# Kernel optimization log

Hardware: AMD Instinct MI355X
Metric: run time of the kernel (lower is better)

The kernel has to match this reference:

```python
import jax, jax.numpy as jnp
import numpy as np


def setup_inputs() -> dict:
    key = jax.random.key(0)
    k1, k2 = jax.random.split(key)
    x = jax.random.normal(k1, (32, 64, 64, 64), dtype=jnp.float32)
    codebook = jax.random.normal(k2, (1024, 64), dtype=jnp.float32)
    return {"x": x, "codebook": codebook}


def reference(x, codebook):
    # x: (B, D, H, W)  codebook: (K, D)
    B, D = x.shape[0], x.shape[1]
    spatial = x.shape[2:]
    flat = x.reshape(B, D, -1).transpose(0, 2, 1)  # (B, N, D)
    dot = jnp.einsum("bnd,kd->bnk", flat, codebook)
    cb_norm = jnp.sum(codebook * codebook, axis=-1)  # (K,)
    indices = jnp.argmin(cb_norm[None, None, :] - 2.0 * dot, axis=-1)  # (B, N)
    quantized = codebook[indices]  # (B, N, D) gather
    out = quantized.transpose(0, 2, 1).reshape(x.shape)
    return out, indices.reshape((B,) + spatial)
```

## Files before the change

kernel.cpp:

```cpp
#include <hip/hip_runtime.h>


typedef _Float16 f16x8 __attribute__((ext_vector_type(8)));
typedef float    f32x4 __attribute__((ext_vector_type(4)));

#define VQ_D    64
#define VQ_HW   4096
#define VQ_NPOS 131072
#define SC      2048.0f
#define EPS_Q   24
#define WS_CBN  65536
#define WS_CNQ  66560
#define WS_CBT  67584
#define WS_CNT  133120
#define WS_LIST 133124

__global__ __launch_bounds__(256)
void vq_prep(const float* __restrict__ cb, float* __restrict__ ws)
{
    const int tid = threadIdx.x;
    const int blk = blockIdx.x;
    if (blk < 64) {
        const int it   = blk * 256 + tid;
        const int ct   = it >> 8;
        const int s    = (it >> 6) & 3;
        const int lane = it & 63;
        const int ks   = s & 1, isR = s >> 1;
        const int n    = ct * 16 + (lane & 15);
        const int k0   = ks * 32 + (lane >> 4) * 8;
        const float* src = cb + n * 64 + k0;
        f16x8 o;
        #pragma unroll
        for (int j = 0; j < 8; ++j) {
            const float b = src[j];
            const _Float16 bh = (_Float16)b;
            o[j] = isR ? (_Float16)((b - (float)bh) * (-2.0f * SC))
                       : (_Float16)(-2.0f * (float)bh);
        }
        ((f16x8*)ws)[it] = o;
    } else if (blk < 128) {
        const int it = (blk - 64) * 256 + tid;
        const int k = it >> 4, j4 = it & 15;
        ((float4*)(ws + WS_CBT))[j4 * 1024 + k] = ((const float4*)cb)[it];
    } else {
        const int k = (blk - 128) * 256 + tid;
        const float4* row = (const float4*)(cb + k * 64);
        float a0 = 0.f, a1 = 0.f, a2 = 0.f, a3 = 0.f;
        #pragma unroll
        for (int j = 0; j < 16; ++j) {
            const float4 c = row[j];
            a0 = fmaf(c.x, c.x, a0); a1 = fmaf(c.y, c.y, a1);
            a2 = fmaf(c.z, c.z, a2); a3 = fmaf(c.w, c.w, a3);
        }
        const float cn = (a0 + a1) + (a2 + a3);
        ws[WS_CBN + k] = cn;
        ws[WS_CNQ + k] = cn * 2048.0f;
        if (k == 0) ((int*)ws)[WS_CNT] = 0;
    }
}

#define GLOAD_LDS(GP, LP)                                                     \
    __builtin_amdgcn_global_load_lds(                                         \
        (const __attribute__((address_space(1))) unsigned int*)(GP),          \
        (__attribute__((address_space(3))) unsigned int*)(LP), 16, 0, 0)

#define STAGE2(CK, BOFF)                                                      \
    {                                                                         \
        const char* gs_ = (const char*)ws + (size_t)(CK) * 8192               \
                          + wv * 2048 + lane * 16;                            \
        char* ld_ = (char*)bbuf + (BOFF) + wv * 2048;                         \
        GLOAD_LDS(gs_, ld_);                                                  \
        GLOAD_LDS(gs_ + 1024, ld_ + 1024);                                    \
    }

#define CT_BODY(BOFF, CI, CTG)                                                \
    {                                                                         \
        const f16x8 B0 = *(const f16x8*)(lp + (BOFF) + (CI) * 4096);          \
        const f16x8 B1 = *(const f16x8*)(lp + (BOFF) + (CI) * 4096 + 1024);   \
        const f16x8 R0 = *(const f16x8*)(lp + (BOFF) + (CI) * 4096 + 2048);   \
        const f16x8 R1 = *(const f16x8*)(lp + (BOFF) + (CI) * 4096 + 3072);   \
        const float cvq = cnq_lds[(CTG) * 16 + m];                            \
        const f32x4 Ci = {cvq, cvq, cvq, cvq};                                \
        f32x4 pa[4], pb[4];                                                   \
        __builtin_amdgcn_s_setprio(1);                                        \
        _Pragma("unroll")                                                     \
        for (int tl = 0; tl < 4; ++tl) {                                      \
            pa[tl] = __builtin_amdgcn_mfma_f32_16x16x32_f16(Ak[tl][0], B0, Ci,    0,0,0); \
            pb[tl] = __builtin_amdgcn_mfma_f32_16x16x32_f16(Ak[tl][1], B1, zero4, 0,0,0); \
        }                                                                     \
        _Pragma("unroll")                                                     \
        for (int tl = 0; tl < 4; ++tl) {                                      \
            pa[tl] = __builtin_amdgcn_mfma_f32_16x16x32_f16(Ah[tl][0], R0, pa[tl], 0,0,0); \
            pb[tl] = __builtin_amdgcn_mfma_f32_16x16x32_f16(Ah[tl][1], R1, pb[tl], 0,0,0); \
        }                                                                     \
        _Pragma("unroll")                                                     \
        for (int tl = 0; tl < 4; ++tl) {                                      \
            pa[tl] = __builtin_amdgcn_mfma_f32_16x16x32_f16(Ra[tl][0], B0, pa[tl], 0,0,0); \
            pb[tl] = __builtin_amdgcn_mfma_f32_16x16x32_f16(Ra[tl][1], B1, pb[tl], 0,0,0); \
        }                                                                     \
        __builtin_amdgcn_s_setprio(0);                                        \
        const int cbase_ = (CTG) * 16 + m;                                    \
        _Pragma("unroll")                                                     \
        for (int tl = 0; tl < 4; ++tl)                                        \
            _Pragma("unroll")                                                 \
            for (int r = 0; r < 4; ++r) {                                     \
                const float q_ = pa[tl][r] + pb[tl][r];                       \
                const int k_ = ((int)q_ << 10) | cbase_;                      \
                int md_;                                                      \
                asm("v_med3_i32 %0, %1, %2, %3"                               \
                    : "=v"(md_) : "v"(k_), "v"(d1[tl][r]), "v"(d2[tl][r]));   \
                d2[tl][r] = md_;                                              \
                d1[tl][r] = (k_ < d1[tl][r]) ? k_ : d1[tl][r];                \
            }                                                                 \
    }

#define ITER_T(VMSTR, DOSTAGE, T)                                             \
    {                                                                         \
        asm volatile("s_waitcnt " VMSTR ::: "memory");                        \
        __builtin_amdgcn_s_barrier();                                         \
        if (DOSTAGE) STAGE2((T) + 3, (((T) + 3) & 3) * 8192)                  \
        const int base_ = ((T) & 3) * 8192;                                   \
        CT_BODY(base_, 0, (T) * 2)                                            \
        CT_BODY(base_, 1, (T) * 2 + 1)                                        \
    }

__global__ __launch_bounds__(256, 2)
void vq_main(const float* __restrict__ x,
             const float* __restrict__ cb,
             float* __restrict__ ws,
             float* __restrict__ out,
             float* __restrict__ idx_out)
{
    __shared__ f16x8 bbuf[4 * 512];
    __shared__ float cnq_lds[1024];
    __shared__ int   sk[256];
    __shared__ int   smg[256];

    const int tid  = threadIdx.x;
    const int lane = tid & 63;
    const int wv   = tid >> 6;
    const int m    = lane & 15;
    const int q    = lane >> 4;

    const int p0 = blockIdx.x * 256;
    const int b  = p0 >> 12;
    const int n0 = p0 & (VQ_HW - 1);
    const float* xw = x + (size_t)b * (VQ_D * VQ_HW) + n0 + wv * 64;

    STAGE2(0, 0)
    STAGE2(1, 8192)
    STAGE2(2, 16384)

    ((float4*)cnq_lds)[tid] = ((const float4*)(ws + WS_CNQ))[tid];

    f16x8 Ah[4][2], Ak[4][2], Ra[4][2];
    #pragma unroll
    for (int tl = 0; tl < 4; ++tl)
        #pragma unroll
        for (int ks = 0; ks < 2; ++ks) {
            f16x8 h8, k8, r8;
            #pragma unroll
            for (int j = 0; j < 8; ++j) {
                const float v = xw[(size_t)(ks * 32 + q * 8 + j) * VQ_HW + tl * 16 + m];
                const _Float16 vh = (_Float16)v;
                h8[j] = vh;
                k8[j] = (_Float16)((float)vh * 2048.0f);
                r8[j] = (_Float16)((v - (float)vh) * SC);
            }
            Ah[tl][ks] = h8; Ak[tl][ks] = k8; Ra[tl][ks] = r8;
        }

    int d1[4][4], d2[4][4];
    #pragma unroll
    for (int tl = 0; tl < 4; ++tl)
        #pragma unroll
        for (int r = 0; r < 4; ++r) { d1[tl][r] = 0x7FFFFFFF; d2[tl][r] = 0x7FFFFFFF; }

    const f32x4 zero4 = {0.f, 0.f, 0.f, 0.f};
    const char* lp = (const char*)bbuf + lane * 16;

    __syncthreads();

    for (int t = 0; t < 29; ++t)
        ITER_T("vmcnt(4)", 1, t)
    ITER_T("vmcnt(4)", 0, 29)
    ITER_T("vmcnt(2)", 0, 30)
    ITER_T("vmcnt(0)", 0, 31)

    #pragma unroll
    for (int off = 1; off < 16; off <<= 1)
        #pragma unroll
        for (int tl = 0; tl < 4; ++tl)
            #pragma unroll
            for (int r = 0; r < 4; ++r) {
                const int od1 = __shfl_xor(d1[tl][r], off, 64);
                const int od2 = __shfl_xor(d2[tl][r], off, 64);
                const int mx  = (d1[tl][r] > od1) ? d1[tl][r] : od1;
                const int mn2 = (d2[tl][r] < od2) ? d2[tl][r] : od2;
                d2[tl][r] = (mx < mn2) ? mx : mn2;
                d1[tl][r] = (d1[tl][r] < od1) ? d1[tl][r] : od1;
            }

    if (m == 0) {
        #pragma unroll
        for (int tl = 0; tl < 4; ++tl)
            #pragma unroll
            for (int r = 0; r < 4; ++r) {
                const int li = wv * 64 + tl * 16 + q * 4 + r;
                sk[li]  = d1[tl][r] & 1023;
                smg[li] = (d2[tl][r] >> 10) - (d1[tl][r] >> 10);
            }
    }
    __syncthreads();

    const int bk = sk[tid];
    idx_out[p0 + tid] = (float)bk;
    if (smg[tid] < EPS_Q) {
        const int slot = atomicAdd((int*)ws + WS_CNT, 1);
        ((int*)ws)[WS_LIST + slot] = p0 + tid;
    }
    const float4* cr = (const float4*)(cb + (size_t)bk * VQ_D);
    float* ob = out + (size_t)b * (VQ_D * VQ_HW) + n0 + tid;
    #pragma unroll
    for (int d4 = 0; d4 < 16; ++d4) {
        const float4 v = cr[d4];
        ob[(size_t)(d4 * 4 + 0) * VQ_HW] = v.x;
        ob[(size_t)(d4 * 4 + 1) * VQ_HW] = v.y;
        ob[(size_t)(d4 * 4 + 2) * VQ_HW] = v.z;
        ob[(size_t)(d4 * 4 + 3) * VQ_HW] = v.w;
    }
}

__global__ __launch_bounds__(64)
void vq_rescan(const float* __restrict__ x,
               const float* __restrict__ cb,
               const float* __restrict__ ws,
               float* __restrict__ out,
               float* __restrict__ idx_out)
{
    __shared__ float xs[VQ_D];
    const int lane = threadIdx.x;
    const int cnt  = ((const int*)ws)[WS_CNT];
    const int* list = (const int*)ws + WS_LIST;
    const float*  cnb  = ws + WS_CBN;
    const float4* cbT4 = (const float4*)(ws + WS_CBT);

    for (int i = blockIdx.x; i < cnt; i += gridDim.x) {
        const int p = list[i];
        const int b = p >> 12, n = p & (VQ_HW - 1);
        xs[lane] = x[(size_t)b * (VQ_D * VQ_HW) + (size_t)lane * VQ_HW + n];
        __syncthreads();
        float4 xr[16];
        #pragma unroll
        for (int j = 0; j < 16; ++j) xr[j] = ((const float4*)xs)[j];

        float bd = 3.4e38f; int bk = 0;
        #pragma unroll 4
        for (int t = 0; t < 16; ++t) {
            const int code = t * 64 + lane;
            float a0 = 0.f, a1 = 0.f, a2 = 0.f, a3 = 0.f;
            #pragma unroll
            for (int j4 = 0; j4 < 16; ++j4) {
                const float4 c = cbT4[j4 * 1024 + code];
                a0 = fmaf(xr[j4].x, c.x, a0); a1 = fmaf(xr[j4].y, c.y, a1);
                a2 = fmaf(xr[j4].z, c.z, a2); a3 = fmaf(xr[j4].w, c.w, a3);
            }
            const float dist = fmaf(-2.0f, (a0 + a1) + (a2 + a3), cnb[code]);
            if (dist < bd) { bd = dist; bk = code; }
        }
        #pragma unroll
        for (int off = 1; off < 64; off <<= 1) {
            const float od = __shfl_xor(bd, off, 64);
            const int   ok = __shfl_xor(bk, off, 64);
            if (od < bd || (od == bd && ok < bk)) { bd = od; bk = ok; }
        }
        out[(size_t)b * (VQ_D * VQ_HW) + (size_t)lane * VQ_HW + n] = cb[(size_t)bk * VQ_D + lane];
        if (lane == 0) idx_out[p] = (float)bk;
        __syncthreads();
    }
}

extern "C" void kernel_launch(void* const* d_in, const int* in_sizes, int n_in,
                              void* d_out, int out_size, void* d_ws, size_t ws_size,
                              hipStream_t stream) {
    const float* x  = (const float*)d_in[0];
    const float* cb = (const float*)d_in[1];
    float* out = (float*)d_out;
    float* idx = out + (size_t)VQ_NPOS * VQ_D;
    float* ws  = (float*)d_ws;

    vq_prep  <<<dim3(132),  dim3(256), 0, stream>>>(cb, ws);
    vq_main  <<<dim3(512),  dim3(256), 0, stream>>>(x, cb, ws, out, idx);
    vq_rescan<<<dim3(1024), dim3(64),  0, stream>>>(x, cb, ws, out, idx);
}
```

Before: 155.5 us.

## Fuse codebook prep into main kernel with global flag spin-wait

The separate codebook preprocessing kernel is folded into the first 132 blocks of the main kernel. Those blocks signal completion through an atomic counter, and every block waits on it only after loading its x tile, which overlaps the prep work with the x loads and removes one kernel launch. A memset clears the flag before launch. The rescan grid is also cut from 1024 to 256 blocks, which may change coverage. The spin-wait assumes all 512 blocks can be co-resident, otherwise it risks deadlock.

```diff
diff --git a/kernel.cpp b/kernel.cpp
--- a/kernel.cpp
+++ b/kernel.cpp
@@ -14,50 +14,7 @@
 #define WS_CBT  67584
 #define WS_CNT  133120
 #define WS_LIST 133124
-
-__global__ __launch_bounds__(256)
-void vq_prep(const float* __restrict__ cb, float* __restrict__ ws)
-{
-    const int tid = threadIdx.x;
-    const int blk = blockIdx.x;
-    if (blk < 64) {
-        const int it   = blk * 256 + tid;
-        const int ct   = it >> 8;
-        const int s    = (it >> 6) & 3;
-        const int lane = it & 63;
-        const int ks   = s & 1, isR = s >> 1;
-        const int n    = ct * 16 + (lane & 15);
-        const int k0   = ks * 32 + (lane >> 4) * 8;
-        const float* src = cb + n * 64 + k0;
-        f16x8 o;
-        #pragma unroll
-        for (int j = 0; j < 8; ++j) {
-            const float b = src[j];
-            const _Float16 bh = (_Float16)b;
-            o[j] = isR ? (_Float16)((b - (float)bh) * (-2.0f * SC))
-                       : (_Float16)(-2.0f * (float)bh);
-        }
-        ((f16x8*)ws)[it] = o;
-    } else if (blk < 128) {
-        const int it = (blk - 64) * 256 + tid;
-        const int k = it >> 4, j4 = it & 15;
-        ((float4*)(ws + WS_CBT))[j4 * 1024 + k] = ((const float4*)cb)[it];
-    } else {
-        const int k = (blk - 128) * 256 + tid;
-        const float4* row = (const float4*)(cb + k * 64);
-        float a0 = 0.f, a1 = 0.f, a2 = 0.f, a3 = 0.f;
-        #pragma unroll
-        for (int j = 0; j < 16; ++j) {
-            const float4 c = row[j];
-            a0 = fmaf(c.x, c.x, a0); a1 = fmaf(c.y, c.y, a1);
-            a2 = fmaf(c.z, c.z, a2); a3 = fmaf(c.w, c.w, a3);
-        }
-        const float cn = (a0 + a1) + (a2 + a3);
-        ws[WS_CBN + k] = cn;
-        ws[WS_CNQ + k] = cn * 2048.0f;
-        if (k == 0) ((int*)ws)[WS_CNT] = 0;
-    }
-}
+#define WS_FLAG 264196
 
 #define GLOAD_LDS(GP, LP)                                                     \
     __builtin_amdgcn_global_load_lds(                                         \
@@ -141,17 +98,57 @@
     const int wv   = tid >> 6;
     const int m    = lane & 15;
     const int q    = lane >> 4;
-
-    const int p0 = blockIdx.x * 256;
+    const int bid  = blockIdx.x;
+
+    if (bid < 64) {
+        const int it   = bid * 256 + tid;
+        const int ct   = it >> 8;
+        const int s    = (it >> 6) & 3;
+        const int ln   = it & 63;
+        const int ks   = s & 1, isR = s >> 1;
+        const int n    = ct * 16 + (ln & 15);
+        const int k0   = ks * 32 + (ln >> 4) * 8;
+        const float* src = cb + n * 64 + k0;
+        f16x8 o;
+        #pragma unroll
+        for (int j = 0; j < 8; ++j) {
+            const float bv = src[j];
+            const _Float16 bh = (_Float16)bv;
+            o[j] = isR ? (_Float16)((bv - (float)bh) * (-2.0f * SC))
+                       : (_Float16)(-2.0f * (float)bh);
+        }
+        ((f16x8*)ws)[it] = o;
+    } else if (bid < 128) {
+        const int it = (bid - 64) * 256 + tid;
+        const int k = it >> 4, j4 = it & 15;
+        ((float4*)(ws + WS_CBT))[j4 * 1024 + k] = ((const float4*)cb)[it];
+    } else if (bid < 132) {
+        const int k = (bid - 128) * 256 + tid;
+        const float4* row = (const float4*)(cb + k * 64);
+        float a0 = 0.f, a1 = 0.f, a2 = 0.f, a3 = 0.f;
+        #pragma unroll
+        for (int j = 0; j < 16; ++j) {
+            const float4 c = row[j];
+            a0 = fmaf(c.x, c.x, a0); a1 = fmaf(c.y, c.y, a1);
+            a2 = fmaf(c.z, c.z, a2); a3 = fmaf(c.w, c.w, a3);
+        }
+        const float cn = (a0 + a1) + (a2 + a3);
+        ws[WS_CBN + k] = cn;
+        ws[WS_CNQ + k] = cn * 2048.0f;
+        if (k == 0) ((int*)ws)[WS_CNT] = 0;
+    }
+    if (bid < 132) {
+        __syncthreads();
+        if (tid == 0) {
+            __threadfence();
+            atomicAdd((int*)ws + WS_FLAG, 1);
+        }
+    }
+
+    const int p0 = bid * 256;
     const int b  = p0 >> 12;
     const int n0 = p0 & (VQ_HW - 1);
     const float* xw = x + (size_t)b * (VQ_D * VQ_HW) + n0 + wv * 64;
-
-    STAGE2(0, 0)
-    STAGE2(1, 8192)
-    STAGE2(2, 16384)
-
-    ((float4*)cnq_lds)[tid] = ((const float4*)(ws + WS_CNQ))[tid];
 
     f16x8 Ah[4][2], Ak[4][2], Ra[4][2];
     #pragma unroll
@@ -169,6 +166,17 @@
             }
             Ah[tl][ks] = h8; Ak[tl][ks] = k8; Ra[tl][ks] = r8;
         }
+
+    if (tid == 0) {
+        while (atomicAdd((int*)ws + WS_FLAG, 0) < 132)
+            __builtin_amdgcn_s_sleep(2);
+    }
+    __syncthreads();
+
+    STAGE2(0, 0)
+    STAGE2(1, 8192)
+    STAGE2(2, 16384)
+    ((float4*)cnq_lds)[tid] = ((const float4*)(ws + WS_CNQ))[tid];
 
     int d1[4][4], d2[4][4];
     #pragma unroll
@@ -289,7 +297,7 @@
     float* idx = out + (size_t)VQ_NPOS * VQ_D;
     float* ws  = (float*)d_ws;
 
-    vq_prep  <<<dim3(132),  dim3(256), 0, stream>>>(cb, ws);
-    vq_main  <<<dim3(512),  dim3(256), 0, stream>>>(x, cb, ws, out, idx);
-    vq_rescan<<<dim3(1024), dim3(64),  0, stream>>>(x, cb, ws, out, idx);
+    hipMemsetAsync((char*)d_ws + (size_t)WS_FLAG * 4, 0, 4, stream);
+    vq_main  <<<dim3(512), dim3(256), 0, stream>>>(x, cb, ws, out, idx);
+    vq_rescan<<<dim3(256), dim3(64),  0, stream>>>(x, cb, ws, out, idx);
 }
```

New measurement: 179.2 us. 1.15x slower.

## Give each wave a private double-buffered codebook ring to drop block barriers

Applied to the files above, without the earlier changes.

Replaces the block-shared 4-slot codebook staging ring, where each wave loaded a quarter of every chunk and a block barrier ran per chunk, with a private 2-slot ring per wave. Each wave now loads the full 8 KB chunk itself and waits only on its own vmcnt, so no s_barrier is needed in the main loop. The cost is four times the global-to-LDS traffic (each wave fetches every chunk), double the LDS footprint (64 KB ring), and a shallower prefetch of one chunk ahead. It also moves the codebook-norm load and the first staging after the x conversion.

```diff
diff --git a/kernel.cpp b/kernel.cpp
--- a/kernel.cpp
+++ b/kernel.cpp
@@ -64,13 +64,14 @@
         (const __attribute__((address_space(1))) unsigned int*)(GP),          \
         (__attribute__((address_space(3))) unsigned int*)(LP), 16, 0, 0)
 
-#define STAGE2(CK, BOFF)                                                      \
+#define STAGEW(CK, SLOT)                                                      \
     {                                                                         \
-        const char* gs_ = (const char*)ws + (size_t)(CK) * 8192               \
-                          + wv * 2048 + lane * 16;                            \
-        char* ld_ = (char*)bbuf + (BOFF) + wv * 2048;                         \
-        GLOAD_LDS(gs_, ld_);                                                  \
-        GLOAD_LDS(gs_ + 1024, ld_ + 1024);                                    \
+        const char* gs_ = (const char*)ws + (size_t)(CK) * 8192 + lane * 16;  \
+        char* ld_ = myring + (SLOT) * 8192;                                   \
+        GLOAD_LDS(gs_,        ld_);        GLOAD_LDS(gs_ + 1024, ld_ + 1024); \
+        GLOAD_LDS(gs_ + 2048, ld_ + 2048); GLOAD_LDS(gs_ + 3072, ld_ + 3072); \
+        GLOAD_LDS(gs_ + 4096, ld_ + 4096); GLOAD_LDS(gs_ + 5120, ld_ + 5120); \
+        GLOAD_LDS(gs_ + 6144, ld_ + 6144); GLOAD_LDS(gs_ + 7168, ld_ + 7168); \
     }
 
 #define CT_BODY(BOFF, CI, CTG)                                                \
@@ -114,16 +115,6 @@
             }                                                                 \
     }
 
-#define ITER_T(VMSTR, DOSTAGE, T)                                             \
-    {                                                                         \
-        asm volatile("s_waitcnt " VMSTR ::: "memory");                        \
-        __builtin_amdgcn_s_barrier();                                         \
-        if (DOSTAGE) STAGE2((T) + 3, (((T) + 3) & 3) * 8192)                  \
-        const int base_ = ((T) & 3) * 8192;                                   \
-        CT_BODY(base_, 0, (T) * 2)                                            \
-        CT_BODY(base_, 1, (T) * 2 + 1)                                        \
-    }
-
 __global__ __launch_bounds__(256, 2)
 void vq_main(const float* __restrict__ x,
              const float* __restrict__ cb,
@@ -131,7 +122,7 @@
              float* __restrict__ out,
              float* __restrict__ idx_out)
 {
-    __shared__ f16x8 bbuf[4 * 512];
+    __shared__ f16x8 bbuf[4 * 1024];
     __shared__ float cnq_lds[1024];
     __shared__ int   sk[256];
     __shared__ int   smg[256];
@@ -147,11 +138,7 @@
     const int n0 = p0 & (VQ_HW - 1);
     const float* xw = x + (size_t)b * (VQ_D * VQ_HW) + n0 + wv * 64;
 
-    STAGE2(0, 0)
-    STAGE2(1, 8192)
-    STAGE2(2, 16384)
-
-    ((float4*)cnq_lds)[tid] = ((const float4*)(ws + WS_CNQ))[tid];
+    char* myring = (char*)bbuf + wv * 16384;
 
     f16x8 Ah[4][2], Ak[4][2], Ra[4][2];
     #pragma unroll
@@ -170,6 +157,9 @@
             Ah[tl][ks] = h8; Ak[tl][ks] = k8; Ra[tl][ks] = r8;
         }
 
+    ((float4*)cnq_lds)[tid] = ((const float4*)(ws + WS_CNQ))[tid];
+    __syncthreads();
+
     int d1[4][4], d2[4][4];
     #pragma unroll
     for (int tl = 0; tl < 4; ++tl)
@@ -177,15 +167,19 @@
         for (int r = 0; r < 4; ++r) { d1[tl][r] = 0x7FFFFFFF; d2[tl][r] = 0x7FFFFFFF; }
 
     const f32x4 zero4 = {0.f, 0.f, 0.f, 0.f};
-    const char* lp = (const char*)bbuf + lane * 16;
-
-    __syncthreads();
-
-    for (int t = 0; t < 29; ++t)
-        ITER_T("vmcnt(4)", 1, t)
-    ITER_T("vmcnt(4)", 0, 29)
-    ITER_T("vmcnt(2)", 0, 30)
-    ITER_T("vmcnt(0)", 0, 31)
+    const char* lp = (const char*)bbuf + wv * 16384 + lane * 16;
+
+    STAGEW(0, 0)
+    for (int t = 0; t < 31; ++t) {
+        STAGEW(t + 1, (t + 1) & 1)
+        asm volatile("s_waitcnt vmcnt(8)" ::: "memory");
+        const int base_ = (t & 1) * 8192;
+        CT_BODY(base_, 0, t * 2)
+        CT_BODY(base_, 1, t * 2 + 1)
+    }
+    asm volatile("s_waitcnt vmcnt(0)" ::: "memory");
+    CT_BODY(8192, 0, 62)
+    CT_BODY(8192, 1, 63)
 
     #pragma unroll
     for (int off = 1; off < 16; off <<= 1)
```

Result: slower. 159.5 us (+2.6%).

## Fuse exact fp32 rescan of ambiguous positions into main kernel

Applied to the files above, without the earlier changes.

Removes the separate rescan kernel and its global atomic work list. Each main block now collects its low-margin positions in an LDS list and rescans them in fp32 per wavefront at the end of the block. This saves a kernel launch and the global atomic traffic. In exchange, blocks with many ambiguous positions take longer and create tail imbalance, and the per-wave LDS staging reuses bbuf without a barrier.

```diff
diff --git a/kernel.cpp b/kernel.cpp
--- a/kernel.cpp
+++ b/kernel.cpp
@@ -12,8 +12,6 @@
 #define WS_CBN  65536
 #define WS_CNQ  66560
 #define WS_CBT  67584
-#define WS_CNT  133120
-#define WS_LIST 133124
 
 __global__ __launch_bounds__(256)
 void vq_prep(const float* __restrict__ cb, float* __restrict__ ws)
@@ -55,7 +53,6 @@
         const float cn = (a0 + a1) + (a2 + a3);
         ws[WS_CBN + k] = cn;
         ws[WS_CNQ + k] = cn * 2048.0f;
-        if (k == 0) ((int*)ws)[WS_CNT] = 0;
     }
 }
 
@@ -135,6 +132,8 @@
     __shared__ float cnq_lds[1024];
     __shared__ int   sk[256];
     __shared__ int   smg[256];
+    __shared__ int   lpos[256];
+    __shared__ int   lcnt;
 
     const int tid  = threadIdx.x;
     const int lane = tid & 63;
@@ -211,72 +210,66 @@
                 smg[li] = (d2[tl][r] >> 10) - (d1[tl][r] >> 10);
             }
     }
+    if (tid == 0) lcnt = 0;
     __syncthreads();
 
     const int bk = sk[tid];
     idx_out[p0 + tid] = (float)bk;
+    {
+        const float4* cr = (const float4*)(cb + (size_t)bk * VQ_D);
+        float* ob = out + (size_t)b * (VQ_D * VQ_HW) + n0 + tid;
+        #pragma unroll
+        for (int d4 = 0; d4 < 16; ++d4) {
+            const float4 v = cr[d4];
+            ob[(size_t)(d4 * 4 + 0) * VQ_HW] = v.x;
+            ob[(size_t)(d4 * 4 + 1) * VQ_HW] = v.y;
+            ob[(size_t)(d4 * 4 + 2) * VQ_HW] = v.z;
+            ob[(size_t)(d4 * 4 + 3) * VQ_HW] = v.w;
+        }
+    }
     if (smg[tid] < EPS_Q) {
-        const int slot = atomicAdd((int*)ws + WS_CNT, 1);
-        ((int*)ws)[WS_LIST + slot] = p0 + tid;
-    }
-    const float4* cr = (const float4*)(cb + (size_t)bk * VQ_D);
-    float* ob = out + (size_t)b * (VQ_D * VQ_HW) + n0 + tid;
-    #pragma unroll
-    for (int d4 = 0; d4 < 16; ++d4) {
-        const float4 v = cr[d4];
-        ob[(size_t)(d4 * 4 + 0) * VQ_HW] = v.x;
-        ob[(size_t)(d4 * 4 + 1) * VQ_HW] = v.y;
-        ob[(size_t)(d4 * 4 + 2) * VQ_HW] = v.z;
-        ob[(size_t)(d4 * 4 + 3) * VQ_HW] = v.w;
-    }
-}
-
-__global__ __launch_bounds__(64)
-void vq_rescan(const float* __restrict__ x,
-               const float* __restrict__ cb,
-               const float* __restrict__ ws,
-               float* __restrict__ out,
-               float* __restrict__ idx_out)
-{
-    __shared__ float xs[VQ_D];
-    const int lane = threadIdx.x;
-    const int cnt  = ((const int*)ws)[WS_CNT];
-    const int* list = (const int*)ws + WS_LIST;
-    const float*  cnb  = ws + WS_CBN;
-    const float4* cbT4 = (const float4*)(ws + WS_CBT);
-
-    for (int i = blockIdx.x; i < cnt; i += gridDim.x) {
-        const int p = list[i];
-        const int b = p >> 12, n = p & (VQ_HW - 1);
-        xs[lane] = x[(size_t)b * (VQ_D * VQ_HW) + (size_t)lane * VQ_HW + n];
-        __syncthreads();
-        float4 xr[16];
-        #pragma unroll
-        for (int j = 0; j < 16; ++j) xr[j] = ((const float4*)xs)[j];
-
-        float bd = 3.4e38f; int bk = 0;
-        #pragma unroll 4
-        for (int t = 0; t < 16; ++t) {
-            const int code = t * 64 + lane;
-            float a0 = 0.f, a1 = 0.f, a2 = 0.f, a3 = 0.f;
-            #pragma unroll
-            for (int j4 = 0; j4 < 16; ++j4) {
-                const float4 c = cbT4[j4 * 1024 + code];
-                a0 = fmaf(xr[j4].x, c.x, a0); a1 = fmaf(xr[j4].y, c.y, a1);
-                a2 = fmaf(xr[j4].z, c.z, a2); a3 = fmaf(xr[j4].w, c.w, a3);
-            }
-            const float dist = fmaf(-2.0f, (a0 + a1) + (a2 + a3), cnb[code]);
-            if (dist < bd) { bd = dist; bk = code; }
-        }
-        #pragma unroll
-        for (int off = 1; off < 64; off <<= 1) {
-            const float od = __shfl_xor(bd, off, 64);
-            const int   ok = __shfl_xor(bk, off, 64);
-            if (od < bd || (od == bd && ok < bk)) { bd = od; bk = ok; }
-        }
-        out[(size_t)b * (VQ_D * VQ_HW) + (size_t)lane * VQ_HW + n] = cb[(size_t)bk * VQ_D + lane];
-        if (lane == 0) idx_out[p] = (float)bk;
-        __syncthreads();
+        const int s_ = atomicAdd(&lcnt, 1);
+        lpos[s_] = tid;
+    }
+    __syncthreads();
+
+    const int nf = lcnt;
+    if (nf > 0) {
+        const float*  cnb  = ws + WS_CBN;
+        const float4* cbT4 = (const float4*)(ws + WS_CBT);
+        float* xsw = (float*)((char*)bbuf + wv * 1024);
+        for (int i = wv; i < nf; i += 4) {
+            const int pos = lpos[i];
+            const int nn  = n0 + pos;
+            xsw[lane] = x[(size_t)b * (VQ_D * VQ_HW) + (size_t)lane * VQ_HW + nn];
+            float4 xr[16];
+            #pragma unroll
+            for (int j = 0; j < 16; ++j) xr[j] = ((const float4*)xsw)[j];
+
+            float bd = 3.4e38f; int bk2 = 0;
+            #pragma unroll 4
+            for (int t = 0; t < 16; ++t) {
+                const int code = t * 64 + lane;
+                float a0 = 0.f, a1 = 0.f, a2 = 0.f, a3 = 0.f;
+                #pragma unroll
+                for (int j4 = 0; j4 < 16; ++j4) {
+                    const float4 c = cbT4[j4 * 1024 + code];
+                    a0 = fmaf(xr[j4].x, c.x, a0); a1 = fmaf(xr[j4].y, c.y, a1);
+                    a2 = fmaf(xr[j4].z, c.z, a2); a3 = fmaf(xr[j4].w, c.w, a3);
+                }
+                const float dist = fmaf(-2.0f, (a0 + a1) + (a2 + a3), cnb[code]);
+                if (dist < bd) { bd = dist; bk2 = code; }
+            }
+            #pragma unroll
+            for (int off = 1; off < 64; off <<= 1) {
+                const float od = __shfl_xor(bd, off, 64);
+                const int   ok = __shfl_xor(bk2, off, 64);
+                if (od < bd || (od == bd && ok < bk2)) { bd = od; bk2 = ok; }
+            }
+            out[(size_t)b * (VQ_D * VQ_HW) + (size_t)lane * VQ_HW + nn] =
+                cb[(size_t)bk2 * VQ_D + lane];
+            if (lane == 0) idx_out[p0 + pos] = (float)bk2;
+        }
     }
 }
 
@@ -289,7 +282,6 @@
     float* idx = out + (size_t)VQ_NPOS * VQ_D;
     float* ws  = (float*)d_ws;
 
-    vq_prep  <<<dim3(132),  dim3(256), 0, stream>>>(cb, ws);
-    vq_main  <<<dim3(512),  dim3(256), 0, stream>>>(x, cb, ws, out, idx);
-    vq_rescan<<<dim3(1024), dim3(64),  0, stream>>>(x, cb, ws, out, idx);
+    vq_prep<<<dim3(132), dim3(256), 0, stream>>>(cb, ws);
+    vq_main<<<dim3(512), dim3(256), 0, stream>>>(x, cb, ws, out, idx);
 }
```

New measurement: 140.9 us. -9.4%, faster.
